# Optimization experiments

Measured on AMD Instinct MI355X. Metric: run time of the kernel, lower is better.

Reference implementation:

```python
import jax, jax.numpy as jnp
import numpy as np

IN_FEATS = 16
OUT_FEATS = 16
EDGE_FEATS = 16
N_NODES = 50000
N_EDGES = 800000


def setup_inputs() -> dict:
    key = jax.random.key(0)
    k = jax.random.split(key, 7)
    feat = jax.random.normal(k[0], (N_NODES, IN_FEATS), dtype=jnp.float32)
    efeat = jax.random.normal(k[1], (N_EDGES, EDGE_FEATS), dtype=jnp.float32)
    # edge_nn = Linear(EDGE_FEATS, IN_FEATS*OUT_FEATS)
    We = jax.random.normal(k[2], (EDGE_FEATS, IN_FEATS * OUT_FEATS), dtype=jnp.float32) * 0.1
    be = jax.random.normal(k[3], (IN_FEATS * OUT_FEATS,), dtype=jnp.float32) * 0.1
    bias = jax.random.normal(k[4], (OUT_FEATS,), dtype=jnp.float32) * 0.1
    src = jax.random.randint(k[5], (N_EDGES,), 0, N_NODES, dtype=jnp.int64 if jax.config.jax_enable_x64 else jnp.int32)
    dst = jnp.sort(jax.random.randint(k[6], (N_EDGES,), 0, N_NODES, dtype=jnp.int64 if jax.config.jax_enable_x64 else jnp.int32))
    return {"feat": feat, "efeat": efeat, "We": We, "be": be, "bias": bias,
            "src": src, "dst": dst, "num_nodes": N_NODES}


def reference(feat, efeat, We, be, bias, src, dst, num_nodes):
    # edge-conditioned weights: [E, in, out]
    w = (efeat @ We + be).reshape(-1, IN_FEATS, OUT_FEATS)
    # gather source features and per-edge matvec: sum_i h_src[e,i] * w[e,i,o]
    m = jnp.einsum('ei,eio->eo', feat[src], w)  # [E, out]
    # segment-sum aggregation to destination nodes ('sum' reducer)
    neigh = jax.ops.segment_sum(m, dst, num_segments=num_nodes)  # [N, out]
    # residual (Identity since in_feats == out_feats) + bias
    return neigh + feat + bias
```

## Files before the change

kernel.cpp:

```cpp
#include <hip/hip_runtime.h>

typedef __attribute__((ext_vector_type(2))) _Float16 half2v;
typedef __attribute__((ext_vector_type(8))) _Float16 half8v;
typedef __attribute__((ext_vector_type(4))) float f32x4;

#define NBLK 2048
#define WT (NBLK * 4)
#define WP_ELEMS (9 * 4 * 16 * 8)
#define RP_OFF 16384
#define MS_OFF (16384 + 262144)

__global__ __launch_bounds__(256) void setup_kernel(
    const float* __restrict__ We, const float* __restrict__ be,
    const int* __restrict__ dst,
    unsigned short* __restrict__ wp, int* __restrict__ rp,
    int E, int N) {
  int idx = blockIdx.x * 256 + threadIdx.x;
  if (idx < WP_ELEMS) {
    int j = idx & 7, n = (idx >> 3) & 15, gg = (idx >> 7) & 3, t = idx >> 9;
    float v = 0.f;
    if (t < 8) {
      int c = (gg >> 1) * 8 + t;
      int i = (gg & 1) * 8 + j;
      v = We[c * 256 + i * 16 + n];
    } else if (gg < 2) {
      v = be[(gg * 8 + j) * 16 + n];
    }
    _Float16 hv = (_Float16)v;
    wp[idx] = __builtin_bit_cast(unsigned short, hv);
  }
  if (idx <= N) {
    int lo = 0, hi = E;
    while (lo < hi) {
      int mid = (lo + hi) >> 1;
      if (dst[mid] < idx) lo = mid + 1; else hi = mid;
    }
    rp[idx] = lo;
  }
}

__device__ __forceinline__ void compute_store(
    unsigned short* __restrict__ ms, int tile,
    float4 E0, float4 E1, float4 H0, float4 H1, bool valid,
    int g, int lane, const half8v* Bf) {
  if (!valid) {
    E0 = make_float4(0.f, 0.f, 0.f, 0.f); E1 = E0; H0 = E0; H1 = E0;
  }
  half2v ef2[4], h2[4];
  ef2[0] = half2v{(_Float16)E0.x, (_Float16)E0.y};
  ef2[1] = half2v{(_Float16)E0.z, (_Float16)E0.w};
  ef2[2] = half2v{(_Float16)E1.x, (_Float16)E1.y};
  ef2[3] = half2v{(_Float16)E1.z, (_Float16)E1.w};
  h2[0]  = half2v{(_Float16)H0.x, (_Float16)H0.y};
  h2[1]  = half2v{(_Float16)H0.z, (_Float16)H0.w};
  h2[2]  = half2v{(_Float16)H1.x, (_Float16)H1.y};
  h2[3]  = half2v{(_Float16)H1.z, (_Float16)H1.w};

  f32x4 accA = {0.f, 0.f, 0.f, 0.f};
  f32x4 accB = {0.f, 0.f, 0.f, 0.f};
#pragma unroll
  for (int t = 0; t < 8; ++t) {
    _Float16 ev = ef2[t >> 1][t & 1];
    half2v evb = half2v{ev, ev};
    half2v a0 = evb * h2[0], a1 = evb * h2[1], a2 = evb * h2[2], a3 = evb * h2[3];
    half8v A;
    A[0] = a0[0]; A[1] = a0[1]; A[2] = a1[0]; A[3] = a1[1];
    A[4] = a2[0]; A[5] = a2[1]; A[6] = a3[0]; A[7] = a3[1];
    if (t & 1)
      accB = __builtin_amdgcn_mfma_f32_16x16x32_f16(A, Bf[t], accB, 0, 0, 0);
    else
      accA = __builtin_amdgcn_mfma_f32_16x16x32_f16(A, Bf[t], accA, 0, 0, 0);
  }
  {
    half2v z = half2v{(_Float16)0.f, (_Float16)0.f};
    half2v b0 = (g < 2) ? h2[0] : z, b1 = (g < 2) ? h2[1] : z;
    half2v b2 = (g < 2) ? h2[2] : z, b3 = (g < 2) ? h2[3] : z;
    half8v A;
    A[0] = b0[0]; A[1] = b0[1]; A[2] = b1[0]; A[3] = b1[1];
    A[4] = b2[0]; A[5] = b2[1]; A[6] = b3[0]; A[7] = b3[1];
    accB = __builtin_amdgcn_mfma_f32_16x16x32_f16(A, Bf[8], accB, 0, 0, 0);
  }
  half2v lo = half2v{(_Float16)(accA[0] + accB[0]), (_Float16)(accA[1] + accB[1])};
  half2v hi = half2v{(_Float16)(accA[2] + accB[2]), (_Float16)(accA[3] + accB[3])};
  uint2 w;
  w.x = __builtin_bit_cast(unsigned, lo);
  w.y = __builtin_bit_cast(unsigned, hi);
  *reinterpret_cast<uint2*>(ms + (size_t)tile * 256 + lane * 4) = w;
}

__global__ __launch_bounds__(256) void edge_gemm_kernel(
    const float* __restrict__ feat, const float* __restrict__ efeat,
    const int* __restrict__ src, const unsigned short* __restrict__ wp,
    unsigned short* __restrict__ ms, int E) {
  int wave = blockIdx.x * 4 + (threadIdx.x >> 6);
  int lane = threadIdx.x & 63;
  int g = lane >> 4, m = lane & 15;
  int p = g >> 1, hh = g & 1;

  int ntiles = (E + 15) >> 4;
  if (wave >= ntiles) return;

  half8v Bf[9];
#pragma unroll
  for (int t = 0; t < 9; ++t)
    Bf[t] = *reinterpret_cast<const half8v*>(wp + (unsigned)(t * 64 + lane) * 8);

  const float4* ef4 = reinterpret_cast<const float4*>(efeat);
  const float4* f4  = reinterpret_cast<const float4*>(feat);

  int tile = wave;
  int e0 = tile * 16 + m;
  bool v_cur = e0 < E;
  int ec0 = min(e0, E - 1);
  float4 E0 = ef4[(unsigned)ec0 * 4 + p * 2];
  float4 E1 = ef4[(unsigned)ec0 * 4 + p * 2 + 1];
  int s0 = src[ec0];
  float4 H0 = f4[(unsigned)s0 * 4 + hh * 2];
  float4 H1 = f4[(unsigned)s0 * 4 + hh * 2 + 1];
  int tile1 = tile + WT;
  int s1 = (tile1 < ntiles) ? src[min(tile1 * 16 + m, E - 1)] : 0;

  while (tile1 < ntiles) {
    int tile2 = tile1 + WT;
    int e1 = tile1 * 16 + m;
    int ec1 = min(e1, E - 1);
    float4 E0n = ef4[(unsigned)ec1 * 4 + p * 2];
    float4 E1n = ef4[(unsigned)ec1 * 4 + p * 2 + 1];
    float4 H0n = f4[(unsigned)s1 * 4 + hh * 2];
    float4 H1n = f4[(unsigned)s1 * 4 + hh * 2 + 1];
    int s2 = src[min(tile2 * 16 + m, E - 1)];
    bool v_n = e1 < E;
    __builtin_amdgcn_sched_barrier(0);

    compute_store(ms, tile, E0, E1, H0, H1, v_cur, g, lane, Bf);

    E0 = E0n; E1 = E1n; H0 = H0n; H1 = H1n; s1 = s2; v_cur = v_n;
    tile = tile1; tile1 = tile2;
  }
  compute_store(ms, tile, E0, E1, H0, H1, v_cur, g, lane, Bf);
}

__device__ __forceinline__ float ms_at(const unsigned short* ms, int e, int c) {
  unsigned short u = ms[((e >> 4) << 8) + (((e >> 2) & 3) << 6) + (c << 2) + (e & 3)];
  return (float)__builtin_bit_cast(_Float16, u);
}

__global__ __launch_bounds__(256) void segsum_kernel(
    const float* __restrict__ feat, const float* __restrict__ bias,
    const unsigned short* __restrict__ ms, const int* __restrict__ rp,
    float* __restrict__ out, int N) {
  int n = blockIdx.x * 16 + (threadIdx.x >> 4);
  int c = threadIdx.x & 15;
  if (n >= N) return;
  int lo = rp[n], hi = rp[n + 1];
  float sum = 0.f;
  int e = lo;
  while (e < hi && (e & 3)) { sum += ms_at(ms, e, c); ++e; }
  while (e + 4 <= hi) {
    const uint2 v = *reinterpret_cast<const uint2*>(
        ms + ((e >> 4) << 8) + (((e >> 2) & 3) << 6) + (c << 2));
    half2v x = __builtin_bit_cast(half2v, v.x);
    half2v y = __builtin_bit_cast(half2v, v.y);
    sum += (float)x[0] + (float)x[1] + (float)y[0] + (float)y[1];
    e += 4;
  }
  while (e < hi) { sum += ms_at(ms, e, c); ++e; }
  out[n * 16 + c] = sum + feat[n * 16 + c] + bias[c];
}

extern "C" void kernel_launch(void* const* d_in, const int* in_sizes, int n_in,
                              void* d_out, int out_size, void* d_ws, size_t ws_size,
                              hipStream_t stream) {
  const float* feat  = (const float*)d_in[0];
  const float* efeat = (const float*)d_in[1];
  const float* We    = (const float*)d_in[2];
  const float* be    = (const float*)d_in[3];
  const float* bias  = (const float*)d_in[4];
  const int*   src   = (const int*)d_in[5];
  const int*   dst   = (const int*)d_in[6];
  float* out = (float*)d_out;

  int E = in_sizes[5];
  int N = out_size / 16;

  unsigned short* wp = (unsigned short*)d_ws;
  int* rp = (int*)((char*)d_ws + RP_OFF);
  unsigned short* ms = (unsigned short*)((char*)d_ws + MS_OFF);

  int setup_items = (N + 1) > WP_ELEMS ? (N + 1) : WP_ELEMS;
  setup_kernel<<<(setup_items + 255) / 256, 256, 0, stream>>>(We, be, dst, wp, rp, E, N);

  int ntiles = (E + 15) / 16;
  int blocksA = min(NBLK, (ntiles + 3) / 4);
  edge_gemm_kernel<<<blocksA, 256, 0, stream>>>(feat, efeat, src, wp, ms, E);

  int blocksB = (N + 15) / 16;
  segsum_kernel<<<blocksB, 256, 0, stream>>>(feat, bias, ms, rp, out, N);
}
```

Baseline: 43.70 us.

## Stage edge and source features through LDS double buffer with coalesced loads

Edge and gathered source-feature loads now use one float4 per lane, so four lanes cover one edge's 16 floats. The values are converted to fp16 once and written to a per-wave double-buffered LDS region, and each lane then reads its MFMA operand fragments back from LDS. The aim is to remove duplicated global loads and conversions, since previously each row was loaded by two lane groups as two float4s. In exchange it adds LDS traffic, a manual vmcnt wait, and relies on implicit wave-level ordering between the LDS writes and the later reads.

```diff
diff --git a/kernel.cpp b/kernel.cpp
--- a/kernel.cpp
+++ b/kernel.cpp
@@ -39,23 +39,33 @@
   }
 }
 
+__device__ __forceinline__ void cvt_mask_write(char* bufb, int lane,
+                                               float4 ve, float4 vh, bool vld) {
+  if (!vld) { ve = make_float4(0.f, 0.f, 0.f, 0.f); vh = ve; }
+  half2v e0 = half2v{(_Float16)ve.x, (_Float16)ve.y};
+  half2v e1 = half2v{(_Float16)ve.z, (_Float16)ve.w};
+  half2v h0 = half2v{(_Float16)vh.x, (_Float16)vh.y};
+  half2v h1 = half2v{(_Float16)vh.z, (_Float16)vh.w};
+  uint2 ew, hw;
+  ew.x = __builtin_bit_cast(unsigned, e0); ew.y = __builtin_bit_cast(unsigned, e1);
+  hw.x = __builtin_bit_cast(unsigned, h0); hw.y = __builtin_bit_cast(unsigned, h1);
+  int el = lane >> 2, q = lane & 3;
+  *reinterpret_cast<uint2*>(bufb + el * 48 + q * 8) = ew;
+  *reinterpret_cast<uint2*>(bufb + 768 + el * 48 + q * 8) = hw;
+}
+
 __device__ __forceinline__ void compute_store(
-    unsigned short* __restrict__ ms, int tile,
-    float4 E0, float4 E1, float4 H0, float4 H1, bool valid,
-    int g, int lane, const half8v* Bf) {
-  if (!valid) {
-    E0 = make_float4(0.f, 0.f, 0.f, 0.f); E1 = E0; H0 = E0; H1 = E0;
-  }
+    unsigned short* __restrict__ ms, int tile, const char* bufb,
+    int g, int m, int lane, const half8v* Bf) {
+  int p = g >> 1, hh = g & 1;
+  half8v efr = *reinterpret_cast<const half8v*>(bufb + m * 48 + p * 16);
+  half8v hfr = *reinterpret_cast<const half8v*>(bufb + 768 + m * 48 + hh * 16);
   half2v ef2[4], h2[4];
-  ef2[0] = half2v{(_Float16)E0.x, (_Float16)E0.y};
-  ef2[1] = half2v{(_Float16)E0.z, (_Float16)E0.w};
-  ef2[2] = half2v{(_Float16)E1.x, (_Float16)E1.y};
-  ef2[3] = half2v{(_Float16)E1.z, (_Float16)E1.w};
-  h2[0]  = half2v{(_Float16)H0.x, (_Float16)H0.y};
-  h2[1]  = half2v{(_Float16)H0.z, (_Float16)H0.w};
-  h2[2]  = half2v{(_Float16)H1.x, (_Float16)H1.y};
-  h2[3]  = half2v{(_Float16)H1.z, (_Float16)H1.w};
-
+#pragma unroll
+  for (int j = 0; j < 4; ++j) {
+    ef2[j] = half2v{efr[2 * j], efr[2 * j + 1]};
+    h2[j]  = half2v{hfr[2 * j], hfr[2 * j + 1]};
+  }
   f32x4 accA = {0.f, 0.f, 0.f, 0.f};
   f32x4 accB = {0.f, 0.f, 0.f, 0.f};
 #pragma unroll
@@ -92,12 +102,14 @@
     const float* __restrict__ feat, const float* __restrict__ efeat,
     const int* __restrict__ src, const unsigned short* __restrict__ wp,
     unsigned short* __restrict__ ms, int E) {
-  int wave = blockIdx.x * 4 + (threadIdx.x >> 6);
+  __shared__ __align__(16) char lds[4][2][1536];
+  int wid = threadIdx.x >> 6;
   int lane = threadIdx.x & 63;
   int g = lane >> 4, m = lane & 15;
-  int p = g >> 1, hh = g & 1;
+  int el = lane >> 2, q = lane & 3;
 
   int ntiles = (E + 15) >> 4;
+  int wave = blockIdx.x * 4 + wid;
   if (wave >= ntiles) return;
 
   half8v Bf[9];
@@ -105,39 +117,36 @@
   for (int t = 0; t < 9; ++t)
     Bf[t] = *reinterpret_cast<const half8v*>(wp + (unsigned)(t * 64 + lane) * 8);
 
-  const float4* ef4 = reinterpret_cast<const float4*>(efeat);
-  const float4* f4  = reinterpret_cast<const float4*>(feat);
-
-  int tile = wave;
-  int e0 = tile * 16 + m;
-  bool v_cur = e0 < E;
-  int ec0 = min(e0, E - 1);
-  float4 E0 = ef4[(unsigned)ec0 * 4 + p * 2];
-  float4 E1 = ef4[(unsigned)ec0 * 4 + p * 2 + 1];
-  int s0 = src[ec0];
-  float4 H0 = f4[(unsigned)s0 * 4 + hh * 2];
-  float4 H1 = f4[(unsigned)s0 * 4 + hh * 2 + 1];
-  int tile1 = tile + WT;
-  int s1 = (tile1 < ntiles) ? src[min(tile1 * 16 + m, E - 1)] : 0;
-
-  while (tile1 < ntiles) {
-    int tile2 = tile1 + WT;
-    int e1 = tile1 * 16 + m;
-    int ec1 = min(e1, E - 1);
-    float4 E0n = ef4[(unsigned)ec1 * 4 + p * 2];
-    float4 E1n = ef4[(unsigned)ec1 * 4 + p * 2 + 1];
-    float4 H0n = f4[(unsigned)s1 * 4 + hh * 2];
-    float4 H1n = f4[(unsigned)s1 * 4 + hh * 2 + 1];
-    int s2 = src[min(tile2 * 16 + m, E - 1)];
-    bool v_n = e1 < E;
+  int t = wave;
+  {
+    int eg = min(t * 16 + el, E - 1);
+    int s  = src[eg];
+    float4 ve = *reinterpret_cast<const float4*>(efeat + (size_t)eg * 16 + q * 4);
+    float4 vh = *reinterpret_cast<const float4*>(feat + (size_t)s * 16 + q * 4);
+    cvt_mask_write(&lds[wid][0][0], lane, ve, vh, (t * 16 + el) < E);
+  }
+  int t1 = t + WT;
+  int s1 = (t1 < ntiles) ? src[min(t1 * 16 + el, E - 1)] : 0;
+  int b = 0;
+
+  while (t1 < ntiles) {
+    int t2 = t1 + WT;
+    int s2 = src[min(min(t2, ntiles - 1) * 16 + el, E - 1)];
+    int eg1 = min(t1 * 16 + el, E - 1);
+    float4 ve = *reinterpret_cast<const float4*>(efeat + (size_t)eg1 * 16 + q * 4);
+    float4 vh = *reinterpret_cast<const float4*>(feat + (size_t)s1 * 16 + q * 4);
     __builtin_amdgcn_sched_barrier(0);
 
-    compute_store(ms, tile, E0, E1, H0, H1, v_cur, g, lane, Bf);
-
-    E0 = E0n; E1 = E1n; H0 = H0n; H1 = H1n; s1 = s2; v_cur = v_n;
-    tile = tile1; tile1 = tile2;
-  }
-  compute_store(ms, tile, E0, E1, H0, H1, v_cur, g, lane, Bf);
+    compute_store(ms, t, &lds[wid][b][0], g, m, lane, Bf);
+
+    asm volatile("s_waitcnt vmcnt(1)" ::: "memory");
+    __builtin_amdgcn_sched_barrier(0);
+    cvt_mask_write(&lds[wid][b ^ 1][0], lane, ve, vh, (t1 * 16 + el) < E);
+
+    s1 = s2;
+    t = t1; t1 = t2; b ^= 1;
+  }
+  compute_store(ms, t, &lds[wid][b][0], g, m, lane, Bf);
 }
 
 __device__ __forceinline__ float ms_at(const unsigned short* ms, int e, int c) {
```

Result: faster. 42.67 us (-2.3%).

## Deepen edge GEMM software pipeline to two tiles ahead with manual waitcnt

Applied to the files above, without the earlier changes.

The edge GEMM kernel now keeps two tiles of edge and source features in flight (plus src indices three tiles ahead) and uses explicit s_waitcnt vmcnt counts so compute on the current tile overlaps the outstanding gathers. The grid is halved to 1024 blocks so each wave handles more tiles and the deeper pipeline can fill. This adds register pressure and relies on hand-chosen vmcnt values matching the number of issued loads and stores, which is fragile.

```diff
diff --git a/kernel.cpp b/kernel.cpp
--- a/kernel.cpp
+++ b/kernel.cpp
@@ -4,8 +4,7 @@
 typedef __attribute__((ext_vector_type(8))) _Float16 half8v;
 typedef __attribute__((ext_vector_type(4))) float f32x4;
 
-#define NBLK 2048
-#define WT (NBLK * 4)
+#define NBLK 1024
 #define WP_ELEMS (9 * 4 * 16 * 8)
 #define RP_OFF 16384
 #define MS_OFF (16384 + 262144)
@@ -92,52 +91,77 @@
     const float* __restrict__ feat, const float* __restrict__ efeat,
     const int* __restrict__ src, const unsigned short* __restrict__ wp,
     unsigned short* __restrict__ ms, int E) {
-  int wave = blockIdx.x * 4 + (threadIdx.x >> 6);
+  int wid = threadIdx.x >> 6;
   int lane = threadIdx.x & 63;
   int g = lane >> 4, m = lane & 15;
   int p = g >> 1, hh = g & 1;
 
   int ntiles = (E + 15) >> 4;
-  if (wave >= ntiles) return;
+  int CW = gridDim.x * 4;
+  int t = blockIdx.x * 4 + wid;
+  if (t >= ntiles) return;
 
   half8v Bf[9];
 #pragma unroll
-  for (int t = 0; t < 9; ++t)
-    Bf[t] = *reinterpret_cast<const half8v*>(wp + (unsigned)(t * 64 + lane) * 8);
+  for (int tt = 0; tt < 9; ++tt)
+    Bf[tt] = *reinterpret_cast<const half8v*>(wp + (unsigned)(tt * 64 + lane) * 8);
 
   const float4* ef4 = reinterpret_cast<const float4*>(efeat);
   const float4* f4  = reinterpret_cast<const float4*>(feat);
 
-  int tile = wave;
-  int e0 = tile * 16 + m;
-  bool v_cur = e0 < E;
-  int ec0 = min(e0, E - 1);
-  float4 E0 = ef4[(unsigned)ec0 * 4 + p * 2];
-  float4 E1 = ef4[(unsigned)ec0 * 4 + p * 2 + 1];
-  int s0 = src[ec0];
-  float4 H0 = f4[(unsigned)s0 * 4 + hh * 2];
-  float4 H1 = f4[(unsigned)s0 * 4 + hh * 2 + 1];
-  int tile1 = tile + WT;
-  int s1 = (tile1 < ntiles) ? src[min(tile1 * 16 + m, E - 1)] : 0;
-
-  while (tile1 < ntiles) {
-    int tile2 = tile1 + WT;
-    int e1 = tile1 * 16 + m;
-    int ec1 = min(e1, E - 1);
-    float4 E0n = ef4[(unsigned)ec1 * 4 + p * 2];
-    float4 E1n = ef4[(unsigned)ec1 * 4 + p * 2 + 1];
-    float4 H0n = f4[(unsigned)s1 * 4 + hh * 2];
-    float4 H1n = f4[(unsigned)s1 * 4 + hh * 2 + 1];
-    int s2 = src[min(tile2 * 16 + m, E - 1)];
-    bool v_n = e1 < E;
+  float4 EA0, EA1, HA0, HA1; bool vA;
+  {
+    int ec = min(t * 16 + m, E - 1); vA = (t * 16 + m) < E;
+    EA0 = ef4[(unsigned)ec * 4 + p * 2]; EA1 = ef4[(unsigned)ec * 4 + p * 2 + 1];
+    int s = src[ec];
+    HA0 = f4[(unsigned)s * 4 + hh * 2]; HA1 = f4[(unsigned)s * 4 + hh * 2 + 1];
+  }
+  int t1 = t + CW;
+  if (t1 >= ntiles) {
+    compute_store(ms, t, EA0, EA1, HA0, HA1, vA, g, lane, Bf);
+    return;
+  }
+  float4 EB0, EB1, HB0, HB1; bool vB;
+  {
+    int ec = min(t1 * 16 + m, E - 1); vB = (t1 * 16 + m) < E;
+    EB0 = ef4[(unsigned)ec * 4 + p * 2]; EB1 = ef4[(unsigned)ec * 4 + p * 2 + 1];
+    int s = src[ec];
+    HB0 = f4[(unsigned)s * 4 + hh * 2]; HB1 = f4[(unsigned)s * 4 + hh * 2 + 1];
+  }
+  int t2 = t1 + CW;
+  int t3 = t2 + CW;
+  int s2 = src[min(min(t2, ntiles - 1) * 16 + m, E - 1)];
+  int s3 = src[min(min(t3, ntiles - 1) * 16 + m, E - 1)];
+  asm volatile("s_waitcnt vmcnt(0)" ::: "memory");
+  __builtin_amdgcn_sched_barrier(0);
+
+  while (t2 < ntiles) {
+    float4 EC0, EC1, HC0, HC1; bool vC;
+    int t4 = t3 + CW;
+    int s4 = src[min(min(t4, ntiles - 1) * 16 + m, E - 1)];
+    {
+      int ec = min(t2 * 16 + m, E - 1); vC = (t2 * 16 + m) < E;
+      EC0 = ef4[(unsigned)ec * 4 + p * 2]; EC1 = ef4[(unsigned)ec * 4 + p * 2 + 1];
+      HC0 = f4[(unsigned)s2 * 4 + hh * 2]; HC1 = f4[(unsigned)s2 * 4 + hh * 2 + 1];
+    }
     __builtin_amdgcn_sched_barrier(0);
 
-    compute_store(ms, tile, E0, E1, H0, H1, v_cur, g, lane, Bf);
-
-    E0 = E0n; E1 = E1n; H0 = H0n; H1 = H1n; s1 = s2; v_cur = v_n;
-    tile = tile1; tile1 = tile2;
-  }
-  compute_store(ms, tile, E0, E1, H0, H1, v_cur, g, lane, Bf);
+    compute_store(ms, t, EA0, EA1, HA0, HA1, vA, g, lane, Bf);
+    __builtin_amdgcn_sched_barrier(0);
+
+    asm volatile("s_waitcnt vmcnt(7)" ::: "memory");
+    __builtin_amdgcn_sched_barrier(0);
+
+    EA0 = EB0; EA1 = EB1; HA0 = HB0; HA1 = HB1; vA = vB;
+    EB0 = EC0; EB1 = EC1; HB0 = HC0; HB1 = HC1; vB = vC;
+    s2 = s3; s3 = s4;
+    t = t1; t1 = t2; t2 = t3; t3 = t4;
+  }
+  asm volatile("s_waitcnt vmcnt(0)" ::: "memory");
+  __builtin_amdgcn_sched_barrier(0);
+  compute_store(ms, t, EA0, EA1, HA0, HA1, vA, g, lane, Bf);
+  if (t1 < ntiles)
+    compute_store(ms, t1, EB0, EB1, HB0, HB1, vB, g, lane, Bf);
 }
 
 __device__ __forceinline__ float ms_at(const unsigned short* ms, int e, int c) {
```

Result: faster. 42.17 us (-3.5%).
